# Optimization experiments

Measured on AMD Instinct MI355X. Metric: run time of the kernel, lower is better.

The kernel has to match this reference:

```python
import jax, jax.numpy as jnp
import numpy as np

N, M, FIN, FOUT, K = 16, 65536, 32, 32, 7


def setup_inputs() -> dict:
    key = jax.random.key(0)
    k1, k2, k3, k4, k5 = jax.random.split(key, 5)
    stdv = 1.0 / np.sqrt(FIN)
    x = jax.random.normal(k1, (N, M, FIN), dtype=jnp.float32)
    weight = jax.random.uniform(k2, (K, FIN, FOUT), dtype=jnp.float32, minval=-stdv, maxval=stdv)
    bias = jax.random.uniform(k3, (FOUT,), dtype=jnp.float32, minval=-stdv, maxval=stdv)
    index_list = jax.random.randint(k4, (M * K,), 0, M, dtype=jnp.int32)
    index_value = jax.random.uniform(k5, (M, K), dtype=jnp.float32)
    return {"x": x, "weight": weight, "bias": bias,
            "index_list": index_list, "index_value": index_value}


def reference(x, weight, bias, index_list, index_value):
    # out[n,m,o] = sum_k sum_f index_value[m,k] * x[n, idx[m,k], f] * weight[k,f,o] + bias[o]
    n, m, fin = x.shape
    k = index_value.shape[1]
    idx = index_list.reshape(m, k)            # [M, K] neighbor ids
    gathered = x[:, idx, :]                    # [N, M, K, Fin] gather of neighbor feats
    weighted = gathered * index_value[None, :, :, None]  # apply adjacency weights
    out = jnp.einsum('nmkf,kfo->nmo', weighted, weight) + bias
    return out
```

## Files before the change

### kernel.cpp

```cpp
#include <hip/hip_runtime.h>
#include <hip/hip_bf16.h>

#define N_    16
#define M_    65536
#define FIN_  32
#define FOUT_ 32
#define K_    7

#define BLOCKS_   2048
#define THREADS_  256
#define WAVES_PB_ 4
#define NXCD_     8
#define WAVES_PER_XCD_ ((BLOCKS_ / NXCD_) * WAVES_PB_)
#define GROUPS_   (M_ / 16)
#define ITERS_    8

typedef __bf16 bf16x8 __attribute__((ext_vector_type(8)));
typedef float  f32x4  __attribute__((ext_vector_type(4)));

__global__ __launch_bounds__(256)
void convert_kernel(const float* __restrict__ x, __bf16* __restrict__ xb)
{
    const size_t tid = (size_t)blockIdx.x * blockDim.x + threadIdx.x;
    const f32x4* src = (const f32x4*)x + tid * 2;
    const f32x4 v0 = __builtin_nontemporal_load(src);
    const f32x4 v1 = __builtin_nontemporal_load(src + 1);
    bf16x8 b;
    #pragma unroll
    for (int j = 0; j < 4; ++j) b[j] = (__bf16)v0[j];
    #pragma unroll
    for (int j = 0; j < 4; ++j) b[4 + j] = (__bf16)v1[j];
    *(bf16x8*)(xb + tid * 8) = b;
}

__global__ __launch_bounds__(256, 4)
void gfc_xcd_kernel(const __bf16* __restrict__ xb,
                    const float* __restrict__ w,
                    const float* __restrict__ bias,
                    const int*   __restrict__ il,
                    const float* __restrict__ iv,
                    float* __restrict__ out)
{
    __shared__ __bf16 wlds[K_ * 2 * 64 * 8];

    const int lane = threadIdx.x & 63;
    const int col  = lane & 15;
    const int kgrp = lane >> 4;

    for (int t = threadIdx.x; t < K_ * 2 * 64; t += THREADS_) {
        const int l  = t & 63;
        const int h  = (t >> 6) & 1;
        const int k  = t >> 7;
        const int c  = l & 15;
        const int kg = l >> 4;
        const float* wp = w + (size_t)k * (FIN_ * FOUT_)
                            + (size_t)(kg * 8) * FOUT_ + h * 16 + c;
        bf16x8 b;
        #pragma unroll
        for (int j = 0; j < 8; ++j) b[j] = (__bf16)wp[j * FOUT_];
        *(bf16x8*)(wlds + (size_t)t * 8) = b;
    }
    __syncthreads();

    const float b_lo = bias[col];
    const float b_hi = bias[16 + col];

    const int xcd  = blockIdx.x & (NXCD_ - 1);
    const int widx = (blockIdx.x >> 3) * WAVES_PB_ + (threadIdx.x >> 6);

    int   idxs[K_];
    float ivs[K_];
    {
        const int m0 = (widx * 4) * 16 + col;
        #pragma unroll
        for (int k = 0; k < K_; ++k) {
            idxs[k] = il[m0 * K_ + k];
            ivs[k]  = iv[m0 * K_ + k];
        }
    }
    bf16x8 raw[K_];
    {
        const __bf16* xn = xb + (size_t)(xcd * 2) * (M_ * FIN_);
        #pragma unroll
        for (int k = 0; k < K_; ++k)
            raw[k] = *(const bf16x8*)(xn + (size_t)idxs[k] * FIN_ + kgrp * 8);
    }

    for (int it = 0; it < ITERS_; ++it) {
        const bool has_next = (it + 1) < ITERS_;

        int   idxn[K_];
        float ivn[K_];
        if (has_next) {
            const int it2 = it + 1;
            const int mn  = (widx * 4 + (it2 & 3)) * 16 + col;
            #pragma unroll
            for (int k = 0; k < K_; ++k) {
                idxn[k] = il[mn * K_ + k];
                ivn[k]  = iv[mn * K_ + k];
            }
        }

        f32x4 acc0 = {0.f, 0.f, 0.f, 0.f};
        f32x4 acc1 = {0.f, 0.f, 0.f, 0.f};
        #pragma unroll
        for (int k = 0; k < K_; ++k) {
            const float ivk = ivs[k];
            bf16x8 a;
            #pragma unroll
            for (int j = 0; j < 8; ++j)
                a[j] = (__bf16)((float)raw[k][j] * ivk);
            const bf16x8 bf0 = *(const bf16x8*)(wlds + ((k * 2 + 0) * 64 + lane) * 8);
            const bf16x8 bf1 = *(const bf16x8*)(wlds + ((k * 2 + 1) * 64 + lane) * 8);
            acc0 = __builtin_amdgcn_mfma_f32_16x16x32_bf16(a, bf0, acc0, 0, 0, 0);
            acc1 = __builtin_amdgcn_mfma_f32_16x16x32_bf16(a, bf1, acc1, 0, 0, 0);
        }

        if (has_next) {
            const int it2 = it + 1;
            const int nn  = xcd * 2 + (it2 >> 2);
            const __bf16* xn = xb + (size_t)nn * (M_ * FIN_);
            #pragma unroll
            for (int k = 0; k < K_; ++k)
                raw[k] = *(const bf16x8*)(xn + (size_t)idxn[k] * FIN_ + kgrp * 8);
            #pragma unroll
            for (int k = 0; k < K_; ++k) { idxs[k] = idxn[k]; ivs[k] = ivn[k]; }
        }

        const int n_cur = xcd * 2 + (it >> 2);
        const int mb    = (widx * 4 + (it & 3)) * 16;
        #pragma unroll
        for (int r = 0; r < 4; ++r) {
            float* op = out + ((size_t)n_cur * M_ + (size_t)(mb + kgrp * 4 + r)) * FOUT_;
            __builtin_nontemporal_store(acc0[r] + b_lo, op + col);
            __builtin_nontemporal_store(acc1[r] + b_hi, op + 16 + col);
        }
    }
}

__global__ __launch_bounds__(256, 4)
void gfc_fallback_kernel(const float* __restrict__ x,
                         const float* __restrict__ w,
                         const float* __restrict__ bias,
                         const int*   __restrict__ index_list,
                         const float* __restrict__ index_value,
                         float* __restrict__ out)
{
    const int lane  = threadIdx.x & 63;
    const int col   = lane & 15;
    const int kgrp  = lane >> 4;

    const int waves_per_block = blockDim.x >> 6;
    const int wave_id     = blockIdx.x * waves_per_block + (threadIdx.x >> 6);
    const int total_waves = gridDim.x * waves_per_block;

    bf16x8 bfrag[K_][2];
    #pragma unroll
    for (int k = 0; k < K_; ++k) {
        #pragma unroll
        for (int h = 0; h < 2; ++h) {
            const float* wp = w + (size_t)k * (FIN_ * FOUT_)
                                + (size_t)(kgrp * 8) * FOUT_ + h * 16 + col;
            bf16x8 b;
            #pragma unroll
            for (int j = 0; j < 8; ++j)
                b[j] = (__bf16)wp[j * FOUT_];
            bfrag[k][h] = b;
        }
    }
    const float b_lo = bias[col];
    const float b_hi = bias[16 + col];

    for (int m = wave_id; m < M_; m += total_waves) {
        f32x4 acc0 = {0.f, 0.f, 0.f, 0.f};
        f32x4 acc1 = {0.f, 0.f, 0.f, 0.f};

        #pragma unroll
        for (int k = 0; k < K_; ++k) {
            const int   m2  = index_list[m * K_ + k];
            const float ivk = index_value[m * K_ + k];
            const float* ap = x + ((size_t)col * M_ + (size_t)m2) * FIN_ + kgrp * 8;
            const float4 v0 = *(const float4*)(ap);
            const float4 v1 = *(const float4*)(ap + 4);
            const float av[8] = {v0.x, v0.y, v0.z, v0.w, v1.x, v1.y, v1.z, v1.w};
            bf16x8 a;
            #pragma unroll
            for (int j = 0; j < 8; ++j)
                a[j] = (__bf16)(av[j] * ivk);
            acc0 = __builtin_amdgcn_mfma_f32_16x16x32_bf16(a, bfrag[k][0], acc0, 0, 0, 0);
            acc1 = __builtin_amdgcn_mfma_f32_16x16x32_bf16(a, bfrag[k][1], acc1, 0, 0, 0);
        }

        #pragma unroll
        for (int r = 0; r < 4; ++r) {
            const int n = kgrp * 4 + r;
            const size_t base = ((size_t)n * M_ + (size_t)m) * FOUT_;
            out[base + col]      = acc0[r] + b_lo;
            out[base + 16 + col] = acc1[r] + b_hi;
        }
    }
}

extern "C" void kernel_launch(void* const* d_in, const int* in_sizes, int n_in,
                              void* d_out, int out_size, void* d_ws, size_t ws_size,
                              hipStream_t stream) {
    const float* x    = (const float*)d_in[0];
    const float* w    = (const float*)d_in[1];
    const float* bias = (const float*)d_in[2];
    const int*   il   = (const int*)  d_in[3];
    const float* iv   = (const float*)d_in[4];
    float* out = (float*)d_out;

    const size_t ws_needed = (size_t)M_ * N_ * FIN_ * sizeof(__bf16);
    if (ws_size >= ws_needed) {
        __bf16* xb = (__bf16*)d_ws;
        const int t_total = N_ * M_ * FIN_ / 8;
        hipLaunchKernelGGL(convert_kernel, dim3(t_total / 256), dim3(256), 0, stream,
                           x, xb);
        hipLaunchKernelGGL(gfc_xcd_kernel, dim3(BLOCKS_), dim3(THREADS_), 0, stream,
                           xb, w, bias, il, iv, out);
    } else {
        hipLaunchKernelGGL(gfc_fallback_kernel, dim3(2048), dim3(256), 0, stream,
                           x, w, bias, il, iv, out);
    }
}
```

Baseline: 340.6 us.

## Interleave batch pairs in bf16 workspace so each gather serves two batches

```diff
diff --git a/kernel.cpp b/kernel.cpp
--- a/kernel.cpp
+++ b/kernel.cpp
@@ -11,35 +11,46 @@
 #define THREADS_  256
 #define WAVES_PB_ 4
 #define NXCD_     8
-#define WAVES_PER_XCD_ ((BLOCKS_ / NXCD_) * WAVES_PB_)
-#define GROUPS_   (M_ / 16)
-#define ITERS_    8
+#define NPAIR_    8
+#define ITERS_    4
 
 typedef __bf16 bf16x8 __attribute__((ext_vector_type(8)));
 typedef float  f32x4  __attribute__((ext_vector_type(4)));
 
 __global__ __launch_bounds__(256)
-void convert_kernel(const float* __restrict__ x, __bf16* __restrict__ xb)
+void convert_pair_kernel(const float* __restrict__ x, __bf16* __restrict__ xb2)
 {
     const size_t tid = (size_t)blockIdx.x * blockDim.x + threadIdx.x;
-    const f32x4* src = (const f32x4*)x + tid * 2;
-    const f32x4 v0 = __builtin_nontemporal_load(src);
-    const f32x4 v1 = __builtin_nontemporal_load(src + 1);
-    bf16x8 b;
-    #pragma unroll
-    for (int j = 0; j < 4; ++j) b[j] = (__bf16)v0[j];
-    #pragma unroll
-    for (int j = 0; j < 4; ++j) b[4 + j] = (__bf16)v1[j];
-    *(bf16x8*)(xb + tid * 8) = b;
+    const int f8 = (int)(tid & 3);
+    const int m  = (int)((tid >> 2) & (M_ - 1));
+    const int p  = (int)(tid >> 18);
+
+    const float* s0 = x + ((size_t)(2 * p) * M_ + m) * FIN_ + f8 * 8;
+    const float* s1 = s0 + (size_t)M_ * FIN_;
+
+    const f32x4 a0 = __builtin_nontemporal_load((const f32x4*)s0);
+    const f32x4 a1 = __builtin_nontemporal_load((const f32x4*)s0 + 1);
+    const f32x4 c0 = __builtin_nontemporal_load((const f32x4*)s1);
+    const f32x4 c1 = __builtin_nontemporal_load((const f32x4*)s1 + 1);
+
+    bf16x8 v0, v1;
+    #pragma unroll
+    for (int j = 0; j < 4; ++j) { v0[j] = (__bf16)a0[j]; v0[4 + j] = (__bf16)a1[j]; }
+    #pragma unroll
+    for (int j = 0; j < 4; ++j) { v1[j] = (__bf16)c0[j]; v1[4 + j] = (__bf16)c1[j]; }
+
+    __bf16* d = xb2 + ((size_t)p * M_ + m) * 64 + f8 * 8;
+    *(bf16x8*)(d)      = v0;
+    *(bf16x8*)(d + 32) = v1;
 }
 
 __global__ __launch_bounds__(256, 4)
-void gfc_xcd_kernel(const __bf16* __restrict__ xb,
-                    const float* __restrict__ w,
-                    const float* __restrict__ bias,
-                    const int*   __restrict__ il,
-                    const float* __restrict__ iv,
-                    float* __restrict__ out)
+void gfc_pair_kernel(const __bf16* __restrict__ xb2,
+                     const float* __restrict__ w,
+                     const float* __restrict__ bias,
+                     const int*   __restrict__ il,
+                     const float* __restrict__ iv,
+                     float* __restrict__ out)
 {
     __shared__ __bf16 wlds[K_ * 2 * 64 * 8];
 
@@ -65,25 +76,26 @@
     const float b_lo = bias[col];
     const float b_hi = bias[16 + col];
 
-    const int xcd  = blockIdx.x & (NXCD_ - 1);
+    const int p    = blockIdx.x & (NXCD_ - 1);
     const int widx = (blockIdx.x >> 3) * WAVES_PB_ + (threadIdx.x >> 6);
+    const __bf16* xp = xb2 + (size_t)p * ((size_t)M_ * 64);
 
     int   idxs[K_];
     float ivs[K_];
     {
-        const int m0 = (widx * 4) * 16 + col;
+        const int m0 = (widx * ITERS_) * 16 + col;
         #pragma unroll
         for (int k = 0; k < K_; ++k) {
             idxs[k] = il[m0 * K_ + k];
             ivs[k]  = iv[m0 * K_ + k];
         }
     }
-    bf16x8 raw[K_];
-    {
-        const __bf16* xn = xb + (size_t)(xcd * 2) * (M_ * FIN_);
-        #pragma unroll
-        for (int k = 0; k < K_; ++k)
-            raw[k] = *(const bf16x8*)(xn + (size_t)idxs[k] * FIN_ + kgrp * 8);
+    bf16x8 raw0[K_], raw1[K_];
+    #pragma unroll
+    for (int k = 0; k < K_; ++k) {
+        const __bf16* g = xp + (size_t)idxs[k] * 64 + kgrp * 8;
+        raw0[k] = *(const bf16x8*)(g);
+        raw1[k] = *(const bf16x8*)(g + 32);
     }
 
     for (int it = 0; it < ITERS_; ++it) {
@@ -92,8 +104,7 @@
         int   idxn[K_];
         float ivn[K_];
         if (has_next) {
-            const int it2 = it + 1;
-            const int mn  = (widx * 4 + (it2 & 3)) * 16 + col;
+            const int mn = (widx * ITERS_ + it + 1) * 16 + col;
             #pragma unroll
             for (int k = 0; k < K_; ++k) {
                 idxn[k] = il[mn * K_ + k];
@@ -101,39 +112,48 @@
             }
         }
 
-        f32x4 acc0 = {0.f, 0.f, 0.f, 0.f};
-        f32x4 acc1 = {0.f, 0.f, 0.f, 0.f};
+        f32x4 acc00 = {0.f, 0.f, 0.f, 0.f};
+        f32x4 acc01 = {0.f, 0.f, 0.f, 0.f};
+        f32x4 acc10 = {0.f, 0.f, 0.f, 0.f};
+        f32x4 acc11 = {0.f, 0.f, 0.f, 0.f};
         #pragma unroll
         for (int k = 0; k < K_; ++k) {
             const float ivk = ivs[k];
-            bf16x8 a;
-            #pragma unroll
-            for (int j = 0; j < 8; ++j)
-                a[j] = (__bf16)((float)raw[k][j] * ivk);
+            bf16x8 a0, a1;
+            #pragma unroll
+            for (int j = 0; j < 8; ++j) {
+                a0[j] = (__bf16)((float)raw0[k][j] * ivk);
+                a1[j] = (__bf16)((float)raw1[k][j] * ivk);
+            }
             const bf16x8 bf0 = *(const bf16x8*)(wlds + ((k * 2 + 0) * 64 + lane) * 8);
             const bf16x8 bf1 = *(const bf16x8*)(wlds + ((k * 2 + 1) * 64 + lane) * 8);
-            acc0 = __builtin_amdgcn_mfma_f32_16x16x32_bf16(a, bf0, acc0, 0, 0, 0);
-            acc1 = __builtin_amdgcn_mfma_f32_16x16x32_bf16(a, bf1, acc1, 0, 0, 0);
+            acc00 = __builtin_amdgcn_mfma_f32_16x16x32_bf16(a0, bf0, acc00, 0, 0, 0);
+            acc01 = __builtin_amdgcn_mfma_f32_16x16x32_bf16(a0, bf1, acc01, 0, 0, 0);
+            acc10 = __builtin_amdgcn_mfma_f32_16x16x32_bf16(a1, bf0, acc10, 0, 0, 0);
+            acc11 = __builtin_amdgcn_mfma_f32_16x16x32_bf16(a1, bf1, acc11, 0, 0, 0);
         }
 
         if (has_next) {
-            const int it2 = it + 1;
-            const int nn  = xcd * 2 + (it2 >> 2);
-            const __bf16* xn = xb + (size_t)nn * (M_ * FIN_);
-            #pragma unroll
-            for (int k = 0; k < K_; ++k)
-                raw[k] = *(const bf16x8*)(xn + (size_t)idxn[k] * FIN_ + kgrp * 8);
+            #pragma unroll
+            for (int k = 0; k < K_; ++k) {
+                const __bf16* g = xp + (size_t)idxn[k] * 64 + kgrp * 8;
+                raw0[k] = *(const bf16x8*)(g);
+                raw1[k] = *(const bf16x8*)(g + 32);
+            }
             #pragma unroll
             for (int k = 0; k < K_; ++k) { idxs[k] = idxn[k]; ivs[k] = ivn[k]; }
         }
 
-        const int n_cur = xcd * 2 + (it >> 2);
-        const int mb    = (widx * 4 + (it & 3)) * 16;
+        const int mb = (widx * ITERS_ + it) * 16;
         #pragma unroll
         for (int r = 0; r < 4; ++r) {
-            float* op = out + ((size_t)n_cur * M_ + (size_t)(mb + kgrp * 4 + r)) * FOUT_;
-            __builtin_nontemporal_store(acc0[r] + b_lo, op + col);
-            __builtin_nontemporal_store(acc1[r] + b_hi, op + 16 + col);
+            const int mrow = mb + kgrp * 4 + r;
+            float* op0 = out + ((size_t)(2 * p)     * M_ + mrow) * FOUT_;
+            float* op1 = out + ((size_t)(2 * p + 1) * M_ + mrow) * FOUT_;
+            __builtin_nontemporal_store(acc00[r] + b_lo, op0 + col);
+            __builtin_nontemporal_store(acc01[r] + b_hi, op0 + 16 + col);
+            __builtin_nontemporal_store(acc10[r] + b_lo, op1 + col);
+            __builtin_nontemporal_store(acc11[r] + b_hi, op1 + 16 + col);
         }
     }
 }
@@ -213,12 +233,12 @@
 
     const size_t ws_needed = (size_t)M_ * N_ * FIN_ * sizeof(__bf16);
     if (ws_size >= ws_needed) {
-        __bf16* xb = (__bf16*)d_ws;
-        const int t_total = N_ * M_ * FIN_ / 8;
-        hipLaunchKernelGGL(convert_kernel, dim3(t_total / 256), dim3(256), 0, stream,
-                           x, xb);
-        hipLaunchKernelGGL(gfc_xcd_kernel, dim3(BLOCKS_), dim3(THREADS_), 0, stream,
-                           xb, w, bias, il, iv, out);
+        __bf16* xb2 = (__bf16*)d_ws;
+        const int t_total = NPAIR_ * M_ * 4;
+        hipLaunchKernelGGL(convert_pair_kernel, dim3(t_total / 256), dim3(256), 0, stream,
+                           x, xb2);
+        hipLaunchKernelGGL(gfc_pair_kernel, dim3(BLOCKS_), dim3(THREADS_), 0, stream,
+                           xb2, w, bias, il, iv, out);
     } else {
         hipLaunchKernelGGL(gfc_fallback_kernel, dim3(2048), dim3(256), 0, stream,
                            x, w, bias, il, iv, out);
```

After: 377.8 us. 10.9% more time.

## Schedule work per XCD via hardware XCC id and atomic chunk tickets across two launches

Applied to the files above, without the earlier changes.

```diff
diff --git a/kernel.cpp b/kernel.cpp
--- a/kernel.cpp
+++ b/kernel.cpp
@@ -9,18 +9,20 @@
 
 #define BLOCKS_   2048
 #define THREADS_  256
-#define WAVES_PB_ 4
-#define NXCD_     8
-#define WAVES_PER_XCD_ ((BLOCKS_ / NXCD_) * WAVES_PB_)
-#define GROUPS_   (M_ / 16)
-#define ITERS_    8
+#define CHUNK_M_  256
+#define CHUNKS_   (M_ / CHUNK_M_)
+#define ITERS_C_  4
 
 typedef __bf16 bf16x8 __attribute__((ext_vector_type(8)));
 typedef float  f32x4  __attribute__((ext_vector_type(4)));
+
+__device__ int g_tickets[16];
 
 __global__ __launch_bounds__(256)
 void convert_kernel(const float* __restrict__ x, __bf16* __restrict__ xb)
 {
+    if (blockIdx.x == 0 && threadIdx.x < 16) g_tickets[threadIdx.x] = 0;
+
     const size_t tid = (size_t)blockIdx.x * blockDim.x + threadIdx.x;
     const f32x4* src = (const f32x4*)x + tid * 2;
     const f32x4 v0 = __builtin_nontemporal_load(src);
@@ -34,18 +36,21 @@
 }
 
 __global__ __launch_bounds__(256, 4)
-void gfc_xcd_kernel(const __bf16* __restrict__ xb,
+void gfc_loc_kernel(const __bf16* __restrict__ xb,
                     const float* __restrict__ w,
                     const float* __restrict__ bias,
                     const int*   __restrict__ il,
                     const float* __restrict__ iv,
-                    float* __restrict__ out)
+                    float* __restrict__ out,
+                    const int launch)
 {
     __shared__ __bf16 wlds[K_ * 2 * 64 * 8];
+    __shared__ int t_sh;
 
     const int lane = threadIdx.x & 63;
     const int col  = lane & 15;
     const int kgrp = lane >> 4;
+    const int wv   = threadIdx.x >> 6;
 
     for (int t = threadIdx.x; t < K_ * 2 * 64; t += THREADS_) {
         const int l  = t & 63;
@@ -65,75 +70,86 @@
     const float b_lo = bias[col];
     const float b_hi = bias[16 + col];
 
-    const int xcd  = blockIdx.x & (NXCD_ - 1);
-    const int widx = (blockIdx.x >> 3) * WAVES_PB_ + (threadIdx.x >> 6);
-
-    int   idxs[K_];
-    float ivs[K_];
-    {
-        const int m0 = (widx * 4) * 16 + col;
-        #pragma unroll
-        for (int k = 0; k < K_; ++k) {
-            idxs[k] = il[m0 * K_ + k];
-            ivs[k]  = iv[m0 * K_ + k];
-        }
-    }
-    bf16x8 raw[K_];
-    {
-        const __bf16* xn = xb + (size_t)(xcd * 2) * (M_ * FIN_);
-        #pragma unroll
-        for (int k = 0; k < K_; ++k)
-            raw[k] = *(const bf16x8*)(xn + (size_t)idxs[k] * FIN_ + kgrp * 8);
-    }
-
-    for (int it = 0; it < ITERS_; ++it) {
-        const bool has_next = (it + 1) < ITERS_;
-
-        int   idxn[K_];
-        float ivn[K_];
-        if (has_next) {
-            const int it2 = it + 1;
-            const int mn  = (widx * 4 + (it2 & 3)) * 16 + col;
+    unsigned xcc_raw;
+    asm volatile("s_getreg_b32 %0, hwreg(HW_REG_XCC_ID, 0, 32)" : "=s"(xcc_raw));
+    const int xcc = (int)(xcc_raw & 7u);
+
+    for (int s = 0; s < 8; ++s) {
+        const int q = (xcc + s) & 7;
+        const int n = launch * 8 + q;
+        const __bf16* xn = xb + ((size_t)n << 21);
+        int* tq = &g_tickets[launch * 8 + q];
+
+        for (;;) {
+            __syncthreads();
+            if (threadIdx.x == 0) t_sh = atomicAdd(tq, 1);
+            __syncthreads();
+            const int t = t_sh;
+            if (t >= CHUNKS_) break;
+
+            const int m_base = t * CHUNK_M_ + wv * 64;
+
+            float ivs[K_];
+            bf16x8 raw[K_];
+            {
+                const int m0 = m_base + col;
+                int idx0[K_];
+                #pragma unroll
+                for (int k = 0; k < K_; ++k) {
+                    idx0[k] = il[m0 * K_ + k];
+                    ivs[k]  = iv[m0 * K_ + k];
+                }
+                #pragma unroll
+                for (int k = 0; k < K_; ++k)
+                    raw[k] = *(const bf16x8*)(xn + (size_t)idx0[k] * FIN_ + kgrp * 8);
+            }
+
             #pragma unroll
-            for (int k = 0; k < K_; ++k) {
-                idxn[k] = il[mn * K_ + k];
-                ivn[k]  = iv[mn * K_ + k];
+            for (int it = 0; it < ITERS_C_; ++it) {
+                const bool hn = (it + 1) < ITERS_C_;
+
+                int   idxn[K_];
+                float ivn[K_];
+                if (hn) {
+                    const int mn = m_base + (it + 1) * 16 + col;
+                    #pragma unroll
+                    for (int k = 0; k < K_; ++k) {
+                        idxn[k] = il[mn * K_ + k];
+                        ivn[k]  = iv[mn * K_ + k];
+                    }
+                }
+
+                f32x4 acc0 = {0.f, 0.f, 0.f, 0.f};
+                f32x4 acc1 = {0.f, 0.f, 0.f, 0.f};
+                #pragma unroll
+                for (int k = 0; k < K_; ++k) {
+                    const float ivk = ivs[k];
+                    bf16x8 a;
+                    #pragma unroll
+                    for (int j = 0; j < 8; ++j)
+                        a[j] = (__bf16)((float)raw[k][j] * ivk);
+                    const bf16x8 bf0 = *(const bf16x8*)(wlds + ((k * 2 + 0) * 64 + lane) * 8);
+                    const bf16x8 bf1 = *(const bf16x8*)(wlds + ((k * 2 + 1) * 64 + lane) * 8);
+                    acc0 = __builtin_amdgcn_mfma_f32_16x16x32_bf16(a, bf0, acc0, 0, 0, 0);
+                    acc1 = __builtin_amdgcn_mfma_f32_16x16x32_bf16(a, bf1, acc1, 0, 0, 0);
+                }
+
+                if (hn) {
+                    #pragma unroll
+                    for (int k = 0; k < K_; ++k)
+                        raw[k] = *(const bf16x8*)(xn + (size_t)idxn[k] * FIN_ + kgrp * 8);
+                    #pragma unroll
+                    for (int k = 0; k < K_; ++k) ivs[k] = ivn[k];
+                }
+
+                const int mb = m_base + it * 16;
+                #pragma unroll
+                for (int r = 0; r < 4; ++r) {
+                    float* op = out + ((size_t)n * M_ + (size_t)(mb + kgrp * 4 + r)) * FOUT_;
+                    __builtin_nontemporal_store(acc0[r] + b_lo, op + col);
+                    __builtin_nontemporal_store(acc1[r] + b_hi, op + 16 + col);
+                }
             }
-        }
-
-        f32x4 acc0 = {0.f, 0.f, 0.f, 0.f};
-        f32x4 acc1 = {0.f, 0.f, 0.f, 0.f};
-        #pragma unroll
-        for (int k = 0; k < K_; ++k) {
-            const float ivk = ivs[k];
-            bf16x8 a;
-            #pragma unroll
-            for (int j = 0; j < 8; ++j)
-                a[j] = (__bf16)((float)raw[k][j] * ivk);
-            const bf16x8 bf0 = *(const bf16x8*)(wlds + ((k * 2 + 0) * 64 + lane) * 8);
-            const bf16x8 bf1 = *(const bf16x8*)(wlds + ((k * 2 + 1) * 64 + lane) * 8);
-            acc0 = __builtin_amdgcn_mfma_f32_16x16x32_bf16(a, bf0, acc0, 0, 0, 0);
-            acc1 = __builtin_amdgcn_mfma_f32_16x16x32_bf16(a, bf1, acc1, 0, 0, 0);
-        }
-
-        if (has_next) {
-            const int it2 = it + 1;
-            const int nn  = xcd * 2 + (it2 >> 2);
-            const __bf16* xn = xb + (size_t)nn * (M_ * FIN_);
-            #pragma unroll
-            for (int k = 0; k < K_; ++k)
-                raw[k] = *(const bf16x8*)(xn + (size_t)idxn[k] * FIN_ + kgrp * 8);
-            #pragma unroll
-            for (int k = 0; k < K_; ++k) { idxs[k] = idxn[k]; ivs[k] = ivn[k]; }
-        }
-
-        const int n_cur = xcd * 2 + (it >> 2);
-        const int mb    = (widx * 4 + (it & 3)) * 16;
-        #pragma unroll
-        for (int r = 0; r < 4; ++r) {
-            float* op = out + ((size_t)n_cur * M_ + (size_t)(mb + kgrp * 4 + r)) * FOUT_;
-            __builtin_nontemporal_store(acc0[r] + b_lo, op + col);
-            __builtin_nontemporal_store(acc1[r] + b_hi, op + 16 + col);
         }
     }
 }
@@ -217,8 +233,10 @@
         const int t_total = N_ * M_ * FIN_ / 8;
         hipLaunchKernelGGL(convert_kernel, dim3(t_total / 256), dim3(256), 0, stream,
                            x, xb);
-        hipLaunchKernelGGL(gfc_xcd_kernel, dim3(BLOCKS_), dim3(THREADS_), 0, stream,
-                           xb, w, bias, il, iv, out);
+        hipLaunchKernelGGL(gfc_loc_kernel, dim3(BLOCKS_), dim3(THREADS_), 0, stream,
+                           xb, w, bias, il, iv, out, 0);
+        hipLaunchKernelGGL(gfc_loc_kernel, dim3(BLOCKS_), dim3(THREADS_), 0, stream,
+                           xb, w, bias, il, iv, out, 1);
     } else {
         hipLaunchKernelGGL(gfc_fallback_kernel, dim3(2048), dim3(256), 0, stream,
                            x, w, bias, il, iv, out);
```

Measured after the change: 577.9 us. 69.7% more time.
